# Kernel optimization log

Hardware: AMD Instinct MI355X
Metric: run time of the kernel (lower is better)

## Reference

```python
import jax, jax.numpy as jnp
import numpy as np

B, T, D_IN, D_H, N_H = 8, 1024, 512, 64, 8
PAD_TAIL = 128


def setup_inputs() -> dict:
    key = jax.random.key(0)
    ks = jax.random.split(key, 7)
    keys = jax.random.normal(ks[0], (B, T, D_IN), jnp.float32)
    queries = jax.random.normal(ks[1], (B, T, D_IN), jnp.float32)
    values = jax.random.normal(ks[2], (B, T, D_IN), jnp.float32)
    # truncated_normal(stddev=0.01) in the original; plain normal*0.01 is a faithful stand-in
    Wk = jax.random.normal(ks[3], (D_IN, D_H, N_H), jnp.float32) * 0.01
    Wq = jax.random.normal(ks[4], (D_IN, D_H, N_H), jnp.float32) * 0.01
    Wv = jax.random.normal(ks[5], (D_IN, D_H, N_H), jnp.float32) * 0.01
    key_seq = jax.random.randint(ks[6], (B, T), 0, 32000)
    key_seq = key_seq.at[:, -PAD_TAIL:].set(-1)  # -1 marks padding positions
    return {"keys": keys, "queries": queries, "values": values,
            "Wk": Wk, "Wq": Wq, "Wv": Wv, "key_seq": key_seq}


def reference(keys, queries, values, Wk, Wq, Wv, key_seq):
    # projections: (b, t, i) x (i, d, h) -> (b, t, d, h)
    Kh = jnp.einsum('bti,idh->btdh', keys, Wk)
    Qh = jnp.einsum('bti,idh->btdh', queries, Wq)
    Vh = jnp.einsum('bti,idh->btdh', values, Wv)

    # scores: i indexes keys, j indexes queries -> (b, Tk, Tq, h)
    scores = jnp.einsum('bidh,bjdh->bijh', Kh, Qh)

    dt = scores.dtype
    # padding mask over key positions (key_seq == -1 -> -1000)
    pad_mask = (-1000.0 * (1.0 - jnp.sign(key_seq + 1).astype(dt)))[:, :, None, None]
    # causal mask: disallow key index i > query index j (matrix_band_part(_, 0, -1) keeps i<=j)
    Tk, Tq = Kh.shape[1], Qh.shape[1]
    caus_mask = -1000.0 * jnp.tril(jnp.ones((Tk, Tq), dt), k=-1)
    mask = pad_mask + caus_mask[None, :, :, None]

    # NB: original adds mask BEFORE scaling, so the -1000 is also scaled. Keep that order.
    hidden_size = Kh.shape[2]
    scores = (scores + mask) / (hidden_size ** 0.5)

    # softmax over the key axis (axis=1)
    attn = jax.nn.softmax(scores, axis=1)

    # aggregate values: (b, i, j, h) x (b, i, d, h) -> (b, j, d, h)
    h_t = jnp.einsum('bijh,bidh->bjdh', attn, Vh)

    # tf.concat(tf.split(h_t, H, axis=-1), axis=2)[:, :, :, 0]
    # == per-head feature blocks laid out head-major along the feature axis
    b, j, d, nh = h_t.shape
    return h_t.transpose(0, 1, 3, 2).reshape(b, j, nh * d)
```

## Files before the change

### kernel.cpp

```cpp
#include <hip/hip_runtime.h>
#include <hip/hip_bf16.h>

#define B_SZ 8
#define T_SZ 1024
#define D_IN 512
#define D_H  64
#define N_H  8

typedef __hip_bfloat16 bf16;
using short8 = __attribute__((ext_vector_type(8))) short;
using short4v = __attribute__((ext_vector_type(4))) short;
using f32x4  = __attribute__((ext_vector_type(4))) float;

__device__ __forceinline__ unsigned short f2bf(float f) {
    union { __hip_bfloat16 b; unsigned short u; } c;
    c.b = __float2bfloat16(f);
    return c.u;
}

__global__ __launch_bounds__(256) void wt_kernel(
    const float* __restrict__ Wk, const float* __restrict__ Wq,
    const float* __restrict__ Wv, unsigned short* __restrict__ Wt)
{
    const int mat = blockIdx.y;
    const float* W = (mat == 0) ? Wk : (mat == 1) ? Wq : Wv;
    int idx = blockIdx.x * 256 + threadIdx.x;
    float v = W[idx];
    int k = idx >> 9, c = idx & 511;
    int h = c & 7, d = c >> 3;
    Wt[(((size_t)mat * 8 + h) * 64 + d) * 512 + k] = f2bf(v);
}

__global__ __launch_bounds__(256) void proj_kernel(
    const float* __restrict__ keys, const float* __restrict__ queries,
    const float* __restrict__ values,
    const unsigned short* __restrict__ Wt, unsigned short* __restrict__ KQVb)
{
    const int tid = threadIdx.x;
    const int m0  = blockIdx.x * 128;
    const int mh  = blockIdx.y;
    const int mat = mh >> 3, h = mh & 7;

    const float* X = (mat == 0) ? keys : (mat == 1) ? queries : values;
    const unsigned short* WT = Wt + (size_t)mh * (64 * 512);
    unsigned short* P = KQVb + (size_t)mat * ((size_t)B_SZ * N_H * T_SZ * D_H);

    __shared__ __align__(16) unsigned short Xst[128 * 72];
    __shared__ __align__(16) unsigned short Wst[64 * 72];

    const int wid = tid >> 6, lane = tid & 63;
    const int quad = lane >> 4, l15 = lane & 15;

    f32x4 acc[2][4];
    #pragma unroll
    for (int a = 0; a < 2; ++a)
        #pragma unroll
        for (int n = 0; n < 4; ++n) acc[a][n] = (f32x4){0.f, 0.f, 0.f, 0.f};

    const float4* X4 = (const float4*)X;

    for (int kc = 0; kc < 8; ++kc) {
        const int k0 = kc * 64;
        __syncthreads();
        #pragma unroll
        for (int q2 = 0; q2 < 8; ++q2) {
            int e = tid + q2 * 256;
            int r = e >> 4, c4 = e & 15;
            float4 v = X4[(size_t)(m0 + r) * (D_IN / 4) + (k0 >> 2) + c4];
            short4v s = {(short)f2bf(v.x), (short)f2bf(v.y),
                         (short)f2bf(v.z), (short)f2bf(v.w)};
            *(short4v*)&Xst[r * 72 + c4 * 4] = s;
        }
        #pragma unroll
        for (int q2 = 0; q2 < 2; ++q2) {
            int e = tid + q2 * 256;
            int d = e >> 3, ch = e & 7;
            *(short8*)&Wst[d * 72 + ch * 8] =
                *(const short8*)&WT[(size_t)d * 512 + k0 + ch * 8];
        }
        __syncthreads();
        #pragma unroll
        for (int ic = 0; ic < 2; ++ic) {
            short8 a0 = *(const short8*)&Xst[(wid*32      + l15) * 72 + ic*32 + quad*8];
            short8 a1 = *(const short8*)&Xst[(wid*32 + 16 + l15) * 72 + ic*32 + quad*8];
            #pragma unroll
            for (int nt = 0; nt < 4; ++nt) {
                short8 bf = *(const short8*)&Wst[(nt*16 + l15) * 72 + ic*32 + quad*8];
                acc[0][nt] = __builtin_amdgcn_mfma_f32_16x16x32_bf16(a0, bf, acc[0][nt], 0, 0, 0);
                acc[1][nt] = __builtin_amdgcn_mfma_f32_16x16x32_bf16(a1, bf, acc[1][nt], 0, 0, 0);
            }
        }
    }

    #pragma unroll
    for (int mt = 0; mt < 2; ++mt)
        #pragma unroll
        for (int r = 0; r < 4; ++r) {
            int m = m0 + wid * 32 + mt * 16 + quad * 4 + r;
            int bb = m >> 10, t = m & 1023;
            size_t base = (((size_t)(bb * N_H + h)) * T_SZ + t) * D_H;
            #pragma unroll
            for (int nt = 0; nt < 4; ++nt)
                P[base + nt * 16 + l15] = f2bf(acc[mt][r >= 0 ? mt : mt][0]),
                P[base + nt * 16 + l15] = f2bf(acc[mt][nt][r]);
        }
}

__global__ __launch_bounds__(256) void attn_kernel(
    const unsigned short* __restrict__ Qb, const unsigned short* __restrict__ Kb,
    const unsigned short* __restrict__ Vb,
    const int* __restrict__ key_seq, float* __restrict__ out)
{
    const int tid = threadIdx.x;
    const int j0  = (int)(gridDim.x - 1 - blockIdx.x) * 64;
    const int h   = blockIdx.y;
    const int b   = blockIdx.z;
    const int wid = tid >> 6, lane = tid & 63;
    const int quad = lane >> 4, l15 = lane & 15;

    __shared__ __align__(16) unsigned short Qst[64 * 72];
    __shared__ __align__(16) unsigned short Kst[64 * 72];
    __shared__ __align__(16) unsigned short VTst[64 * 72];
    __shared__ __align__(16) unsigned short Pst[4][64 * 20];
    __shared__ float spadf[64];

    const size_t bh = (size_t)(b * N_H + h) * T_SZ;

    #pragma unroll
    for (int q2 = 0; q2 < 2; ++q2) {
        int e = tid + q2 * 256;
        int j = e >> 3, ch = e & 7;
        *(short8*)&Qst[j * 72 + ch * 8] =
            *(const short8*)&Qb[(bh + j0 + j) * D_H + ch * 8];
    }
    __syncthreads();
    short8 qf0 = *(const short8*)&Qst[(wid * 16 + l15) * 72 +  0 + quad * 8];
    short8 qf1 = *(const short8*)&Qst[(wid * 16 + l15) * 72 + 32 + quad * 8];

    const int jg = j0 + wid * 16 + l15;

    float m = -1e30f, l = 0.f;
    f32x4 o0 = {0.f,0.f,0.f,0.f}, o1 = o0, o2 = o0, o3 = o0;

    const int ntiles = j0 / 64 + 1;
    for (int it64 = 0; it64 < ntiles; ++it64) {
        const int i0 = it64 * 64;
        __syncthreads();
        #pragma unroll
        for (int q2 = 0; q2 < 2; ++q2) {
            int e = tid + q2 * 256;
            int i = e >> 3, ch = e & 7;
            *(short8*)&Kst[i * 72 + ch * 8] =
                *(const short8*)&Kb[(bh + i0 + i) * D_H + ch * 8];
        }
        #pragma unroll
        for (int q2 = 0; q2 < 2; ++q2) {
            int e = tid + q2 * 256;
            int i = e & 63, ch = e >> 6;
            short8 v = *(const short8*)&Vb[(bh + i0 + i) * D_H + ch * 8];
            #pragma unroll
            for (int c = 0; c < 8; ++c)
                VTst[(ch * 8 + c) * 72 + i] = (unsigned short)v[c];
        }
        if (tid < 64)
            spadf[tid] = (key_seq[b * T_SZ + i0 + tid] == -1) ? -1000.f : 0.f;
        __syncthreads();

        float sv[16];
        #pragma unroll
        for (int it = 0; it < 4; ++it) {
            f32x4 s = {0.f, 0.f, 0.f, 0.f};
            short8 a0 = *(const short8*)&Kst[(it*16 + l15) * 72 +  0 + quad*8];
            s = __builtin_amdgcn_mfma_f32_16x16x32_bf16(a0, qf0, s, 0, 0, 0);
            short8 a1 = *(const short8*)&Kst[(it*16 + l15) * 72 + 32 + quad*8];
            s = __builtin_amdgcn_mfma_f32_16x16x32_bf16(a1, qf1, s, 0, 0, 0);
            #pragma unroll
            for (int r = 0; r < 4; ++r) {
                int iloc = it * 16 + quad * 4 + r;
                float v = s[r] + spadf[iloc];
                if (i0 + iloc > jg) v -= 1000.f;
                sv[it * 4 + r] = v * 0.125f;
            }
        }

        float mt = sv[0];
        #pragma unroll
        for (int k = 1; k < 16; ++k) mt = fmaxf(mt, sv[k]);
        mt = fmaxf(mt, __shfl_xor(mt, 16));
        mt = fmaxf(mt, __shfl_xor(mt, 32));
        const float mnew  = fmaxf(m, mt);
        const float alpha = __expf(m - mnew);
        float p[16], ls = 0.f;
        #pragma unroll
        for (int k = 0; k < 16; ++k) { p[k] = __expf(sv[k] - mnew); ls += p[k]; }
        ls += __shfl_xor(ls, 16);
        ls += __shfl_xor(ls, 32);
        l = l * alpha + ls;
        m = mnew;
        o0 *= alpha; o1 *= alpha; o2 *= alpha; o3 *= alpha;

        #pragma unroll
        for (int it = 0; it < 4; ++it)
            #pragma unroll
            for (int r = 0; r < 4; ++r)
                Pst[wid][(it * 16 + quad * 4 + r) * 20 + l15] =
                    f2bf(p[it * 4 + r]);

        short8 pf0, pf1;
        #pragma unroll
        for (int jj = 0; jj < 8; ++jj) {
            pf0[jj] = (short)Pst[wid][(     quad * 8 + jj) * 20 + l15];
            pf1[jj] = (short)Pst[wid][(32 + quad * 8 + jj) * 20 + l15];
        }

        short8 a;
        a = *(const short8*)&VTst[(     l15) * 72 +      quad * 8];
        o0 = __builtin_amdgcn_mfma_f32_16x16x32_bf16(a, pf0, o0, 0, 0, 0);
        a = *(const short8*)&VTst[(     l15) * 72 + 32 + quad * 8];
        o0 = __builtin_amdgcn_mfma_f32_16x16x32_bf16(a, pf1, o0, 0, 0, 0);
        a = *(const short8*)&VTst[(16 + l15) * 72 +      quad * 8];
        o1 = __builtin_amdgcn_mfma_f32_16x16x32_bf16(a, pf0, o1, 0, 0, 0);
        a = *(const short8*)&VTst[(16 + l15) * 72 + 32 + quad * 8];
        o1 = __builtin_amdgcn_mfma_f32_16x16x32_bf16(a, pf1, o1, 0, 0, 0);
        a = *(const short8*)&VTst[(32 + l15) * 72 +      quad * 8];
        o2 = __builtin_amdgcn_mfma_f32_16x16x32_bf16(a, pf0, o2, 0, 0, 0);
        a = *(const short8*)&VTst[(32 + l15) * 72 + 32 + quad * 8];
        o2 = __builtin_amdgcn_mfma_f32_16x16x32_bf16(a, pf1, o2, 0, 0, 0);
        a = *(const short8*)&VTst[(48 + l15) * 72 +      quad * 8];
        o3 = __builtin_amdgcn_mfma_f32_16x16x32_bf16(a, pf0, o3, 0, 0, 0);
        a = *(const short8*)&VTst[(48 + l15) * 72 + 32 + quad * 8];
        o3 = __builtin_amdgcn_mfma_f32_16x16x32_bf16(a, pf1, o3, 0, 0, 0);
    }

    const float inv = 1.f / l;
    float* op = out + ((size_t)b * T_SZ + jg) * (N_H * D_H) + h * D_H + quad * 4;
    #pragma unroll
    for (int r = 0; r < 4; ++r) {
        op[ 0 + r] = o0[r] * inv;
        op[16 + r] = o1[r] * inv;
        op[32 + r] = o2[r] * inv;
        op[48 + r] = o3[r] * inv;
    }
}

extern "C" void kernel_launch(void* const* d_in, const int* in_sizes, int n_in,
                              void* d_out, int out_size, void* d_ws, size_t ws_size,
                              hipStream_t stream) {
    const float* keys    = (const float*)d_in[0];
    const float* queries = (const float*)d_in[1];
    const float* values  = (const float*)d_in[2];
    const float* Wk      = (const float*)d_in[3];
    const float* Wq      = (const float*)d_in[4];
    const float* Wv      = (const float*)d_in[5];
    const int*   key_seq = (const int*)d_in[6];

    const size_t per = (size_t)B_SZ * N_H * T_SZ * D_H;
    unsigned short* KQVb = (unsigned short*)d_ws;
    unsigned short* Kb = KQVb;
    unsigned short* Qb = KQVb + per;
    unsigned short* Vb = KQVb + 2 * per;
    unsigned short* Wt = KQVb + 3 * per;

    wt_kernel<<<dim3(512 * 512 / 256, 3), 256, 0, stream>>>(Wk, Wq, Wv, Wt);
    proj_kernel<<<dim3((B_SZ * T_SZ) / 128, 3 * N_H), 256, 0, stream>>>(
        keys, queries, values, Wt, KQVb);
    attn_kernel<<<dim3(T_SZ / 64, N_H, B_SZ), 256, 0, stream>>>(
        Qb, Kb, Vb, key_seq, (float*)d_out);
}
```

Before: 183.9 us.

## Restructure projection GEMM tiles, pre-transpose V, and use single-wave attention blocks

```diff
diff --git a/kernel.cpp b/kernel.cpp
--- a/kernel.cpp
+++ b/kernel.cpp
@@ -8,9 +8,9 @@
 #define N_H  8
 
 typedef __hip_bfloat16 bf16;
-using short8 = __attribute__((ext_vector_type(8))) short;
+using short8  = __attribute__((ext_vector_type(8))) short;
 using short4v = __attribute__((ext_vector_type(4))) short;
-using f32x4  = __attribute__((ext_vector_type(4))) float;
+using f32x4   = __attribute__((ext_vector_type(4))) float;
 
 __device__ __forceinline__ unsigned short f2bf(float f) {
     union { __hip_bfloat16 b; unsigned short u; } c;
@@ -18,9 +18,10 @@
     return c.u;
 }
 
-__global__ __launch_bounds__(256) void wt_kernel(
+__global__ __launch_bounds__(256) void prep_kernel(
     const float* __restrict__ Wk, const float* __restrict__ Wq,
-    const float* __restrict__ Wv, unsigned short* __restrict__ Wt)
+    const float* __restrict__ Wv, const int* __restrict__ key_seq,
+    unsigned short* __restrict__ Wt, float* __restrict__ padf)
 {
     const int mat = blockIdx.y;
     const float* W = (mat == 0) ? Wk : (mat == 1) ? Wq : Wv;
@@ -29,6 +30,8 @@
     int k = idx >> 9, c = idx & 511;
     int h = c & 7, d = c >> 3;
     Wt[(((size_t)mat * 8 + h) * 64 + d) * 512 + k] = f2bf(v);
+    if (mat == 2 && idx < B_SZ * T_SZ)
+        padf[idx] = (key_seq[idx] == -1) ? -1000.f : 0.f;
 }
 
 __global__ __launch_bounds__(256) void proj_kernel(
@@ -38,24 +41,25 @@
 {
     const int tid = threadIdx.x;
     const int m0  = blockIdx.x * 128;
-    const int mh  = blockIdx.y;
-    const int mat = mh >> 3, h = mh & 7;
+    const int mat = blockIdx.y >> 2, ntile = blockIdx.y & 3;
+    const int n0  = ntile * 128;
 
     const float* X = (mat == 0) ? keys : (mat == 1) ? queries : values;
-    const unsigned short* WT = Wt + (size_t)mh * (64 * 512);
+    const unsigned short* WTm = Wt + (size_t)mat * 512 * 512;
     unsigned short* P = KQVb + (size_t)mat * ((size_t)B_SZ * N_H * T_SZ * D_H);
 
-    __shared__ __align__(16) unsigned short Xst[128 * 72];
-    __shared__ __align__(16) unsigned short Wst[64 * 72];
+    __shared__ __align__(16) unsigned short Ast[128 * 72];
+    __shared__ __align__(16) unsigned short Bst[128 * 72];
 
     const int wid = tid >> 6, lane = tid & 63;
     const int quad = lane >> 4, l15 = lane & 15;
-
-    f32x4 acc[2][4];
-    #pragma unroll
-    for (int a = 0; a < 2; ++a)
-        #pragma unroll
-        for (int n = 0; n < 4; ++n) acc[a][n] = (f32x4){0.f, 0.f, 0.f, 0.f};
+    const int wm = wid >> 1, wn = wid & 1;
+
+    f32x4 acc[4][4];
+    #pragma unroll
+    for (int i = 0; i < 4; ++i)
+        #pragma unroll
+        for (int j = 0; j < 4; ++j) acc[i][j] = (f32x4){0.f, 0.f, 0.f, 0.f};
 
     const float4* X4 = (const float4*)X;
 
@@ -63,81 +67,104 @@
         const int k0 = kc * 64;
         __syncthreads();
         #pragma unroll
-        for (int q2 = 0; q2 < 8; ++q2) {
-            int e = tid + q2 * 256;
+        for (int q = 0; q < 8; ++q) {
+            int e = tid + q * 256;
             int r = e >> 4, c4 = e & 15;
             float4 v = X4[(size_t)(m0 + r) * (D_IN / 4) + (k0 >> 2) + c4];
             short4v s = {(short)f2bf(v.x), (short)f2bf(v.y),
                          (short)f2bf(v.z), (short)f2bf(v.w)};
-            *(short4v*)&Xst[r * 72 + c4 * 4] = s;
-        }
-        #pragma unroll
-        for (int q2 = 0; q2 < 2; ++q2) {
-            int e = tid + q2 * 256;
-            int d = e >> 3, ch = e & 7;
-            *(short8*)&Wst[d * 72 + ch * 8] =
-                *(const short8*)&WT[(size_t)d * 512 + k0 + ch * 8];
+            *(short4v*)&Ast[r * 72 + c4 * 4] = s;
+        }
+        #pragma unroll
+        for (int q = 0; q < 4; ++q) {
+            int e = tid + q * 256;
+            int r = e >> 3, ch = e & 7;
+            *(short8*)&Bst[r * 72 + ch * 8] =
+                *(const short8*)&WTm[(size_t)(n0 + r) * 512 + k0 + ch * 8];
         }
         __syncthreads();
         #pragma unroll
-        for (int ic = 0; ic < 2; ++ic) {
-            short8 a0 = *(const short8*)&Xst[(wid*32      + l15) * 72 + ic*32 + quad*8];
-            short8 a1 = *(const short8*)&Xst[(wid*32 + 16 + l15) * 72 + ic*32 + quad*8];
+        for (int kc2 = 0; kc2 < 2; ++kc2) {
+            short8 af[4], bfr[4];
+            #pragma unroll
+            for (int mt = 0; mt < 4; ++mt)
+                af[mt] = *(const short8*)&Ast[(wm*64 + mt*16 + l15) * 72 + kc2*32 + quad*8];
+            #pragma unroll
+            for (int nt = 0; nt < 4; ++nt)
+                bfr[nt] = *(const short8*)&Bst[(wn*64 + nt*16 + l15) * 72 + kc2*32 + quad*8];
+            #pragma unroll
+            for (int mt = 0; mt < 4; ++mt)
+                #pragma unroll
+                for (int nt = 0; nt < 4; ++nt)
+                    acc[mt][nt] = __builtin_amdgcn_mfma_f32_16x16x32_bf16(
+                        af[mt], bfr[nt], acc[mt][nt], 0, 0, 0);
+        }
+    }
+
+    #pragma unroll
+    for (int mt = 0; mt < 4; ++mt)
+        #pragma unroll
+        for (int r = 0; r < 4; ++r) {
+            int m = m0 + wm * 64 + mt * 16 + quad * 4 + r;
+            int bb = m >> 10, t = m & 1023;
             #pragma unroll
             for (int nt = 0; nt < 4; ++nt) {
-                short8 bf = *(const short8*)&Wst[(nt*16 + l15) * 72 + ic*32 + quad*8];
-                acc[0][nt] = __builtin_amdgcn_mfma_f32_16x16x32_bf16(a0, bf, acc[0][nt], 0, 0, 0);
-                acc[1][nt] = __builtin_amdgcn_mfma_f32_16x16x32_bf16(a1, bf, acc[1][nt], 0, 0, 0);
+                int n = n0 + wn * 64 + nt * 16 + l15;
+                int h = n >> 6, d = n & 63;
+                P[(((size_t)(bb * 8 + h)) * 1024 + t) * 64 + d] =
+                    f2bf(acc[mt][nt][r]);
             }
         }
-    }
-
-    #pragma unroll
-    for (int mt = 0; mt < 2; ++mt)
-        #pragma unroll
-        for (int r = 0; r < 4; ++r) {
-            int m = m0 + wid * 32 + mt * 16 + quad * 4 + r;
-            int bb = m >> 10, t = m & 1023;
-            size_t base = (((size_t)(bb * N_H + h)) * T_SZ + t) * D_H;
-            #pragma unroll
-            for (int nt = 0; nt < 4; ++nt)
-                P[base + nt * 16 + l15] = f2bf(acc[mt][r >= 0 ? mt : mt][0]),
-                P[base + nt * 16 + l15] = f2bf(acc[mt][nt][r]);
-        }
-}
-
-__global__ __launch_bounds__(256) void attn_kernel(
+}
+
+__global__ __launch_bounds__(256) void vt_kernel(
+    const unsigned short* __restrict__ Vb, unsigned short* __restrict__ Vt)
+{
+    const int tid = threadIdx.x;
+    const int t0  = blockIdx.x * 64;
+    const int bh  = blockIdx.y;
+    __shared__ __align__(16) unsigned short Tst[64 * 72];
+    #pragma unroll
+    for (int q = 0; q < 2; ++q) {
+        int e = tid + q * 256;
+        int t = e >> 3, ch = e & 7;
+        *(short8*)&Tst[t * 72 + ch * 8] =
+            *(const short8*)&Vb[((size_t)bh * T_SZ + t0 + t) * 64 + ch * 8];
+    }
+    __syncthreads();
+    #pragma unroll
+    for (int q = 0; q < 2; ++q) {
+        int e = tid + q * 256;
+        int d = e & 63, ch8 = e >> 6;
+        short8 v;
+        #pragma unroll
+        for (int c = 0; c < 8; ++c) v[c] = (short)Tst[(ch8 * 8 + c) * 72 + d];
+        *(short8*)&Vt[((size_t)bh * 64 + d) * 1024 + t0 + ch8 * 8] = v;
+    }
+}
+
+__global__ __launch_bounds__(64) void attn_kernel(
     const unsigned short* __restrict__ Qb, const unsigned short* __restrict__ Kb,
-    const unsigned short* __restrict__ Vb,
-    const int* __restrict__ key_seq, float* __restrict__ out)
-{
-    const int tid = threadIdx.x;
-    const int j0  = (int)(gridDim.x - 1 - blockIdx.x) * 64;
-    const int h   = blockIdx.y;
-    const int b   = blockIdx.z;
-    const int wid = tid >> 6, lane = tid & 63;
-    const int quad = lane >> 4, l15 = lane & 15;
-
-    __shared__ __align__(16) unsigned short Qst[64 * 72];
-    __shared__ __align__(16) unsigned short Kst[64 * 72];
-    __shared__ __align__(16) unsigned short VTst[64 * 72];
-    __shared__ __align__(16) unsigned short Pst[4][64 * 20];
-    __shared__ float spadf[64];
-
-    const size_t bh = (size_t)(b * N_H + h) * T_SZ;
-
-    #pragma unroll
-    for (int q2 = 0; q2 < 2; ++q2) {
-        int e = tid + q2 * 256;
-        int j = e >> 3, ch = e & 7;
-        *(short8*)&Qst[j * 72 + ch * 8] =
-            *(const short8*)&Qb[(bh + j0 + j) * D_H + ch * 8];
-    }
-    __syncthreads();
-    short8 qf0 = *(const short8*)&Qst[(wid * 16 + l15) * 72 +  0 + quad * 8];
-    short8 qf1 = *(const short8*)&Qst[(wid * 16 + l15) * 72 + 32 + quad * 8];
-
-    const int jg = j0 + wid * 16 + l15;
+    const unsigned short* __restrict__ Vt, const float* __restrict__ padf,
+    float* __restrict__ out)
+{
+    const int x    = blockIdx.x;
+    const int jt16 = 63 - (x >> 6);
+    const int bh6  = x & 63;
+    const int bh   = ((bh6 & 7) << 3) | (bh6 >> 3);
+    const int j0   = jt16 * 16;
+    const int b    = bh >> 3, h = bh & 7;
+    const int lane = threadIdx.x, quad = lane >> 4, l15 = lane & 15;
+
+    __shared__ __align__(16) unsigned short PstT[16 * 72];
+
+    const size_t bhT = (size_t)bh * T_SZ;
+
+    const short8 qf0 = *(const short8*)&Qb[(bhT + j0 + l15) * 64 + quad * 8];
+    const short8 qf1 = *(const short8*)&Qb[(bhT + j0 + l15) * 64 + 32 + quad * 8];
+    const int jg = j0 + l15;
+
+    const float SCALE = 0.125f * 1.44269504088896341f;
 
     float m = -1e30f, l = 0.f;
     f32x4 o0 = {0.f,0.f,0.f,0.f}, o1 = o0, o2 = o0, o3 = o0;
@@ -145,41 +172,23 @@
     const int ntiles = j0 / 64 + 1;
     for (int it64 = 0; it64 < ntiles; ++it64) {
         const int i0 = it64 * 64;
-        __syncthreads();
-        #pragma unroll
-        for (int q2 = 0; q2 < 2; ++q2) {
-            int e = tid + q2 * 256;
-            int i = e >> 3, ch = e & 7;
-            *(short8*)&Kst[i * 72 + ch * 8] =
-                *(const short8*)&Kb[(bh + i0 + i) * D_H + ch * 8];
-        }
-        #pragma unroll
-        for (int q2 = 0; q2 < 2; ++q2) {
-            int e = tid + q2 * 256;
-            int i = e & 63, ch = e >> 6;
-            short8 v = *(const short8*)&Vb[(bh + i0 + i) * D_H + ch * 8];
-            #pragma unroll
-            for (int c = 0; c < 8; ++c)
-                VTst[(ch * 8 + c) * 72 + i] = (unsigned short)v[c];
-        }
-        if (tid < 64)
-            spadf[tid] = (key_seq[b * T_SZ + i0 + tid] == -1) ? -1000.f : 0.f;
-        __syncthreads();
 
         float sv[16];
         #pragma unroll
         for (int it = 0; it < 4; ++it) {
             f32x4 s = {0.f, 0.f, 0.f, 0.f};
-            short8 a0 = *(const short8*)&Kst[(it*16 + l15) * 72 +  0 + quad*8];
+            short8 a0 = *(const short8*)&Kb[(bhT + i0 + it*16 + l15) * 64 + quad * 8];
             s = __builtin_amdgcn_mfma_f32_16x16x32_bf16(a0, qf0, s, 0, 0, 0);
-            short8 a1 = *(const short8*)&Kst[(it*16 + l15) * 72 + 32 + quad*8];
+            short8 a1 = *(const short8*)&Kb[(bhT + i0 + it*16 + l15) * 64 + 32 + quad * 8];
             s = __builtin_amdgcn_mfma_f32_16x16x32_bf16(a1, qf1, s, 0, 0, 0);
+            float4 pd4 = *(const float4*)&padf[b * T_SZ + i0 + it*16 + quad*4];
+            float pdv[4] = {pd4.x, pd4.y, pd4.z, pd4.w};
             #pragma unroll
             for (int r = 0; r < 4; ++r) {
                 int iloc = it * 16 + quad * 4 + r;
-                float v = s[r] + spadf[iloc];
+                float v = s[r] + pdv[r];
                 if (i0 + iloc > jg) v -= 1000.f;
-                sv[it * 4 + r] = v * 0.125f;
+                sv[it * 4 + r] = v * SCALE;
             }
         }
 
@@ -189,10 +198,10 @@
         mt = fmaxf(mt, __shfl_xor(mt, 16));
         mt = fmaxf(mt, __shfl_xor(mt, 32));
         const float mnew  = fmaxf(m, mt);
-        const float alpha = __expf(m - mnew);
+        const float alpha = exp2f(m - mnew);
         float p[16], ls = 0.f;
         #pragma unroll
-        for (int k = 0; k < 16; ++k) { p[k] = __expf(sv[k] - mnew); ls += p[k]; }
+        for (int k = 0; k < 16; ++k) { p[k] = exp2f(sv[k] - mnew); ls += p[k]; }
         ls += __shfl_xor(ls, 16);
         ls += __shfl_xor(ls, 32);
         l = l * alpha + ls;
@@ -200,47 +209,39 @@
         o0 *= alpha; o1 *= alpha; o2 *= alpha; o3 *= alpha;
 
         #pragma unroll
-        for (int it = 0; it < 4; ++it)
-            #pragma unroll
-            for (int r = 0; r < 4; ++r)
-                Pst[wid][(it * 16 + quad * 4 + r) * 20 + l15] =
-                    f2bf(p[it * 4 + r]);
-
-        short8 pf0, pf1;
-        #pragma unroll
-        for (int jj = 0; jj < 8; ++jj) {
-            pf0[jj] = (short)Pst[wid][(     quad * 8 + jj) * 20 + l15];
-            pf1[jj] = (short)Pst[wid][(32 + quad * 8 + jj) * 20 + l15];
-        }
+        for (int it = 0; it < 4; ++it) {
+            short4v pk = {(short)f2bf(p[it*4+0]), (short)f2bf(p[it*4+1]),
+                          (short)f2bf(p[it*4+2]), (short)f2bf(p[it*4+3])};
+            *(short4v*)&PstT[l15 * 72 + it * 16 + quad * 4] = pk;
+        }
+        const short8 pf0 = *(const short8*)&PstT[l15 * 72 + quad * 8];
+        const short8 pf1 = *(const short8*)&PstT[l15 * 72 + 32 + quad * 8];
 
         short8 a;
-        a = *(const short8*)&VTst[(     l15) * 72 +      quad * 8];
+        a = *(const short8*)&Vt[((size_t)bh*64 +  0 + l15) * 1024 + i0 + quad*8];
         o0 = __builtin_amdgcn_mfma_f32_16x16x32_bf16(a, pf0, o0, 0, 0, 0);
-        a = *(const short8*)&VTst[(     l15) * 72 + 32 + quad * 8];
+        a = *(const short8*)&Vt[((size_t)bh*64 +  0 + l15) * 1024 + i0 + 32 + quad*8];
         o0 = __builtin_amdgcn_mfma_f32_16x16x32_bf16(a, pf1, o0, 0, 0, 0);
-        a = *(const short8*)&VTst[(16 + l15) * 72 +      quad * 8];
+        a = *(const short8*)&Vt[((size_t)bh*64 + 16 + l15) * 1024 + i0 + quad*8];
         o1 = __builtin_amdgcn_mfma_f32_16x16x32_bf16(a, pf0, o1, 0, 0, 0);
-        a = *(const short8*)&VTst[(16 + l15) * 72 + 32 + quad * 8];
+        a = *(const short8*)&Vt[((size_t)bh*64 + 16 + l15) * 1024 + i0 + 32 + quad*8];
         o1 = __builtin_amdgcn_mfma_f32_16x16x32_bf16(a, pf1, o1, 0, 0, 0);
-        a = *(const short8*)&VTst[(32 + l15) * 72 +      quad * 8];
+        a = *(const short8*)&Vt[((size_t)bh*64 + 32 + l15) * 1024 + i0 + quad*8];
         o2 = __builtin_amdgcn_mfma_f32_16x16x32_bf16(a, pf0, o2, 0, 0, 0);
-        a = *(const short8*)&VTst[(32 + l15) * 72 + 32 + quad * 8];
+        a = *(const short8*)&Vt[((size_t)bh*64 + 32 + l15) * 1024 + i0 + 32 + quad*8];
         o2 = __builtin_amdgcn_mfma_f32_16x16x32_bf16(a, pf1, o2, 0, 0, 0);
-        a = *(const short8*)&VTst[(48 + l15) * 72 +      quad * 8];
+        a = *(const short8*)&Vt[((size_t)bh*64 + 48 + l15) * 1024 + i0 + quad*8];
         o3 = __builtin_amdgcn_mfma_f32_16x16x32_bf16(a, pf0, o3, 0, 0, 0);
-        a = *(const short8*)&VTst[(48 + l15) * 72 + 32 + quad * 8];
+        a = *(const short8*)&Vt[((size_t)bh*64 + 48 + l15) * 1024 + i0 + 32 + quad*8];
         o3 = __builtin_amdgcn_mfma_f32_16x16x32_bf16(a, pf1, o3, 0, 0, 0);
     }
 
     const float inv = 1.f / l;
     float* op = out + ((size_t)b * T_SZ + jg) * (N_H * D_H) + h * D_H + quad * 4;
-    #pragma unroll
-    for (int r = 0; r < 4; ++r) {
-        op[ 0 + r] = o0[r] * inv;
-        op[16 + r] = o1[r] * inv;
-        op[32 + r] = o2[r] * inv;
-        op[48 + r] = o3[r] * inv;
-    }
+    *(float4*)(op +  0) = (float4){o0[0]*inv, o0[1]*inv, o0[2]*inv, o0[3]*inv};
+    *(float4*)(op + 16) = (float4){o1[0]*inv, o1[1]*inv, o1[2]*inv, o1[3]*inv};
+    *(float4*)(op + 32) = (float4){o2[0]*inv, o2[1]*inv, o2[2]*inv, o2[3]*inv};
+    *(float4*)(op + 48) = (float4){o3[0]*inv, o3[1]*inv, o3[2]*inv, o3[3]*inv};
 }
 
 extern "C" void kernel_launch(void* const* d_in, const int* in_sizes, int n_in,
@@ -255,15 +256,16 @@
     const int*   key_seq = (const int*)d_in[6];
 
     const size_t per = (size_t)B_SZ * N_H * T_SZ * D_H;
-    unsigned short* KQVb = (unsigned short*)d_ws;
-    unsigned short* Kb = KQVb;
-    unsigned short* Qb = KQVb + per;
-    unsigned short* Vb = KQVb + 2 * per;
-    unsigned short* Wt = KQVb + 3 * per;
-
-    wt_kernel<<<dim3(512 * 512 / 256, 3), 256, 0, stream>>>(Wk, Wq, Wv, Wt);
-    proj_kernel<<<dim3((B_SZ * T_SZ) / 128, 3 * N_H), 256, 0, stream>>>(
-        keys, queries, values, Wt, KQVb);
-    attn_kernel<<<dim3(T_SZ / 64, N_H, B_SZ), 256, 0, stream>>>(
-        Qb, Kb, Vb, key_seq, (float*)d_out);
-}
+    unsigned short* Kb = (unsigned short*)d_ws;
+    unsigned short* Qb = Kb + per;
+    unsigned short* Vb = Kb + 2 * per;
+    unsigned short* Vt = Kb + 3 * per;
+    unsigned short* Wt = Kb + 4 * per;
+    float*          padf = (float*)(Wt + 3 * 512 * 512);
+
+    prep_kernel<<<dim3(1024, 3), 256, 0, stream>>>(Wk, Wq, Wv, key_seq, Wt, padf);
+    proj_kernel<<<dim3((B_SZ * T_SZ) / 128, 12), 256, 0, stream>>>(
+        keys, queries, values, Wt, Kb);
+    vt_kernel<<<dim3(16, 64), 256, 0, stream>>>(Vb, Vt);
+    attn_kernel<<<dim3(64 * 64), 64, 0, stream>>>(Qb, Kb, Vt, padf, (float*)d_out);
+}
```

Result: slower. 203.5 us (+10.6%).
